# Kernel tuning notes

Measured on AMD Instinct MI355X. Metric: run time of the kernel, lower is better.

## Reference

```python
import jax, jax.numpy as jnp
import numpy as np

B, N, C, H = 8, 4096, 768, 8
EPS = 1e-12  # F.normalize eps


def setup_inputs() -> dict:
    key = jax.random.key(0)
    k1, k2, k3, k4 = jax.random.split(key, 4)
    x = jax.random.normal(k1, (B, N, C), dtype=jnp.float32)
    Wqkv = jax.random.normal(k2, (C, 3 * C), dtype=jnp.float32) * (1.0 / np.sqrt(C))
    temperature = jnp.ones((H, 1, 1), dtype=jnp.float32)
    Wproj = jax.random.normal(k3, (C, C), dtype=jnp.float32) * (1.0 / np.sqrt(C))
    bproj = jax.random.normal(k4, (C,), dtype=jnp.float32) * 0.01
    return {"x": x, "Wqkv": Wqkv, "temperature": temperature, "Wproj": Wproj, "bproj": bproj}


def _l2norm(t):
    # F.normalize(dim=-1): t / max(||t||_2, eps)
    n = jnp.sqrt(jnp.sum(t * t, axis=-1, keepdims=True))
    return t / jnp.maximum(n, EPS)


def reference(x, Wqkv, temperature, Wproj, bproj):
    b, n, c = x.shape
    h = temperature.shape[0]
    hd = c // h
    qkv = x @ Wqkv  # [B, N, 3C]
    qkv = qkv.reshape(b, n, 3, h, hd).transpose(2, 0, 3, 4, 1)  # [3, B, H, hd, N]
    q, k, v = qkv[0], qkv[1], qkv[2]
    q = _l2norm(q)  # normalize over token dim N
    k = _l2norm(k)
    # channel-channel attention: [B, H, hd, hd]
    attn = jnp.einsum('bhdn,bhen->bhde', q, k) * temperature  # temperature [H,1,1] broadcasts
    attn = jax.nn.softmax(attn, axis=-1)
    out = jnp.einsum('bhde,bhen->bhdn', attn, v)  # [B, H, hd, N]
    out = out.transpose(0, 3, 1, 2).reshape(b, n, c)  # [B, N, C]
    return out @ Wproj + bproj
```

## Files before the change

kernel.cpp:

```cpp
#include <hip/hip_runtime.h>
#include <stdint.h>


typedef __attribute__((ext_vector_type(8))) __bf16 bf16x8;
typedef __attribute__((ext_vector_type(4))) float f32x4;

__device__ __forceinline__ unsigned short f2b(float f) {
  uint32_t u = __float_as_uint(f);
  u += 0x7FFF + ((u >> 16) & 1);
  return (unsigned short)(u >> 16);
}

__device__ __forceinline__ void gload16(const void* g, void* l) {
  __builtin_amdgcn_global_load_lds(
      (__attribute__((address_space(1))) void*)(uintptr_t)g,
      (__attribute__((address_space(3))) void*)(uintptr_t)l, 16, 0, 0);
}

__global__ void cvt_bf16(const float* __restrict__ in, unsigned short* __restrict__ out, int n4,
                         float* __restrict__ Z, int nz4) {
  int gid = blockIdx.x * blockDim.x + threadIdx.x;
  if (gid < nz4) reinterpret_cast<float4*>(Z)[gid] = make_float4(0.f, 0.f, 0.f, 0.f);
  int stride = gridDim.x * blockDim.x;
  for (int i = gid; i < n4; i += stride) {
    float4 v = reinterpret_cast<const float4*>(in)[i];
    ushort4 o;
    o.x = f2b(v.x); o.y = f2b(v.y); o.z = f2b(v.z); o.w = f2b(v.w);
    reinterpret_cast<ushort4*>(out)[i] = o;
  }
}

__global__ void cvt_transpose(const float* __restrict__ in, unsigned short* __restrict__ out,
                              int K, int NC) {
  __shared__ float tile[32][33];
  int bx = blockIdx.x, by = blockIdx.y;
  int tx = threadIdx.x & 31, ty = threadIdx.x >> 5;
  for (int r = ty; r < 32; r += 8)
    tile[r][tx] = in[(size_t)(by * 32 + r) * NC + bx * 32 + tx];
  __syncthreads();
  for (int r = ty; r < 32; r += 8)
    out[(size_t)(bx * 32 + r) * K + by * 32 + tx] = f2b(tile[tx][r]);
}

__global__ __launch_bounds__(256, 2) void gemm_qkv(
    const unsigned short* __restrict__ A, const unsigned short* __restrict__ Bt,
    unsigned short* __restrict__ qkT, unsigned short* __restrict__ vT,
    float* __restrict__ normsq) {
  __shared__ __align__(16) unsigned short lds[17408];
  int bj = blockIdx.x;
  int bm = blockIdx.y;
  int m0 = bm * 128, j0 = bj * 128;
  int tid = threadIdx.x;
  int wid = tid >> 6, lane = tid & 63;
  int wm = wid >> 1, wn = wid & 1;
  int quad = lane >> 4, l16 = lane & 15;
  int srow = lane >> 3, sch = lane & 7;
  int cmem = sch ^ srow;

  f32x4 acc[4][4];
  f32x4 z = {0.f, 0.f, 0.f, 0.f};
#pragma unroll
  for (int i = 0; i < 4; i++)
#pragma unroll
    for (int j = 0; j < 4; j++) acc[i][j] = z;

  const unsigned short* Ab = A + (size_t)m0 * 768;
  const unsigned short* Bb = Bt + (size_t)j0 * 768;

  for (int k0 = 0; k0 < 768; k0 += 64) {
#pragma unroll
    for (int i = 0; i < 4; i++) {
      int ig = wid * 4 + i;
      int row = ig * 8 + srow;
      gload16(Ab + (size_t)row * 768 + k0 + cmem * 8, &lds[ig * 512]);
      gload16(Bb + (size_t)row * 768 + k0 + cmem * 8, &lds[8192 + ig * 512]);
    }
    __syncthreads();
#pragma unroll
    for (int kk = 0; kk < 2; kk++) {
      int cs = ((kk * 4 + quad) ^ (l16 & 7)) * 8;
      bf16x8 af[4], bfr[4];
#pragma unroll
      for (int mi = 0; mi < 4; mi++)
        af[mi] = *(const bf16x8*)&lds[(wm * 64 + mi * 16 + l16) * 64 + cs];
#pragma unroll
      for (int ni = 0; ni < 4; ni++)
        bfr[ni] = *(const bf16x8*)&lds[8192 + (wn * 64 + ni * 16 + l16) * 64 + cs];
#pragma unroll
      for (int mi = 0; mi < 4; mi++)
#pragma unroll
        for (int ni = 0; ni < 4; ni++)
          acc[mi][ni] = __builtin_amdgcn_mfma_f32_16x16x32_bf16(af[mi], bfr[ni], acc[mi][ni], 0, 0, 0);
    }
    __syncthreads();
  }

  int s = bj / 6;
  int b = bm >> 5;
  int n0 = m0 & 4095;
  bool isv = (s == 2);

  if (!isv) {
#pragma unroll
    for (int ni = 0; ni < 4; ni++) {
      float ss = 0.f;
#pragma unroll
      for (int mi = 0; mi < 4; mi++)
#pragma unroll
        for (int r = 0; r < 4; r++) ss += acc[mi][ni][r] * acc[mi][ni][r];
      ss += __shfl_down(ss, 32, 64);
      ss += __shfl_down(ss, 16, 64);
      if (lane < 16) {
        int cc = wn * 64 + ni * 16 + l16;
        int local = j0 + cc - s * 768;
        int hh = local / 96, d = local - hh * 96;
        atomicAdd(&normsq[s * 6144 + (b * 8 + hh) * 96 + d], ss);
      }
    }
  }

#pragma unroll
  for (int mi = 0; mi < 4; mi++)
#pragma unroll
    for (int ni = 0; ni < 4; ni++)
#pragma unroll
      for (int r = 0; r < 4; r++) {
        int m = wm * 64 + mi * 16 + quad * 4 + r;
        int cc = wn * 64 + ni * 16 + l16;
        unsigned short v = f2b(acc[mi][ni][r]);
        lds[isv ? (m * 136 + cc) : (cc * 136 + m)] = v;
      }
  __syncthreads();
  if (!isv) {
#pragma unroll
    for (int it = 0; it < 8; it++) {
      int id = tid + it * 256;
      int jr = id >> 4, mc = id & 15;
      int j = j0 + jr;
      int hh = (j - s * 768) / 96;
      int d = j - s * 768 - hh * 96;
      size_t off = ((size_t)(s * 64 + b * 8 + hh) * 96 + d) * 4096 + n0 + mc * 8;
      *(uint4*)&qkT[off] = *(const uint4*)&lds[jr * 136 + mc * 8];
    }
  } else {
#pragma unroll
    for (int it = 0; it < 8; it++) {
      int id = tid + it * 256;
      int mr = id >> 4, ch = id & 15;
      int cp = (j0 - 1536) + ch * 8;
      int hh = cp / 96, e = cp - hh * 96;
      size_t off = ((size_t)(b * 8 + hh) * 4096 + (n0 + mr)) * 96 + e;
      *(uint4*)&vT[off] = *(const uint4*)&lds[mr * 136 + ch * 8];
    }
  }
}

__global__ __launch_bounds__(256, 2) void attn_s(const unsigned short* __restrict__ qkT,
                                                 float* __restrict__ S) {
  __shared__ __align__(16) unsigned short lds[12288];
  int blk = blockIdx.x;
  int bh = blk >> 3, ks = blk & 7;
  const unsigned short* qb = qkT + (size_t)bh * 96 * 4096;
  const unsigned short* kb = qkT + (size_t)(64 + bh) * 96 * 4096;
  int tid = threadIdx.x, wid = tid >> 6, lane = tid & 63;
  int wm = wid >> 1, wn = wid & 1, quad = lane >> 4, l16 = lane & 15;
  int srow = lane >> 3, sch = lane & 7;
  int cmem = sch ^ srow;
  f32x4 acc[3][3];
  f32x4 z = {0.f, 0.f, 0.f, 0.f};
#pragma unroll
  for (int i = 0; i < 3; i++)
#pragma unroll
    for (int j = 0; j < 3; j++) acc[i][j] = z;

  for (int k0 = ks * 512; k0 < ks * 512 + 512; k0 += 64) {
#pragma unroll
    for (int i = 0; i < 3; i++) {
      int ig = wid * 3 + i;
      int row = ig * 8 + srow;
      gload16(qb + (size_t)row * 4096 + k0 + cmem * 8, &lds[ig * 512]);
      gload16(kb + (size_t)row * 4096 + k0 + cmem * 8, &lds[6144 + ig * 512]);
    }
    __syncthreads();
#pragma unroll
    for (int kk = 0; kk < 2; kk++) {
      int cs = ((kk * 4 + quad) ^ (l16 & 7)) * 8;
      bf16x8 af[3], bfr[3];
#pragma unroll
      for (int mi = 0; mi < 3; mi++)
        af[mi] = *(const bf16x8*)&lds[(wm * 48 + mi * 16 + l16) * 64 + cs];
#pragma unroll
      for (int ni = 0; ni < 3; ni++)
        bfr[ni] = *(const bf16x8*)&lds[6144 + (wn * 48 + ni * 16 + l16) * 64 + cs];
#pragma unroll
      for (int mi = 0; mi < 3; mi++)
#pragma unroll
        for (int ni = 0; ni < 3; ni++)
          acc[mi][ni] = __builtin_amdgcn_mfma_f32_16x16x32_bf16(af[mi], bfr[ni], acc[mi][ni], 0, 0, 0);
    }
    __syncthreads();
  }
  float* Sb = S + (size_t)bh * 9216;
#pragma unroll
  for (int mi = 0; mi < 3; mi++)
#pragma unroll
    for (int ni = 0; ni < 3; ni++)
#pragma unroll
      for (int r = 0; r < 4; r++)
        atomicAdd(&Sb[(wm * 48 + mi * 16 + quad * 4 + r) * 96 + wn * 48 + ni * 16 + l16],
                  acc[mi][ni][r]);
}

__global__ __launch_bounds__(128) void softmax96(
    const float* __restrict__ S, const float* __restrict__ normsq,
    const float* __restrict__ temp, unsigned short* __restrict__ attnB) {
  __shared__ float ik[96];
  int bh = blockIdx.x;
  int h = bh & 7;
  int tid = threadIdx.x;
  if (tid < 96) ik[tid] = 1.0f / fmaxf(sqrtf(normsq[6144 + bh * 96 + tid]), 1e-12f);
  __syncthreads();
  if (tid < 96) {
    int d = tid;
    const float* Srow = S + (size_t)bh * 9216 + d * 96;
    float iq = (1.0f / fmaxf(sqrtf(normsq[bh * 96 + d]), 1e-12f)) * temp[h];
    float mx = -1e30f;
    for (int e = 0; e < 96; e++) mx = fmaxf(mx, Srow[e] * iq * ik[e]);
    float sum = 0.f;
    for (int e = 0; e < 96; e++) sum += __expf(Srow[e] * iq * ik[e] - mx);
    float inv = 1.0f / sum;
    unsigned short* row = attnB + (size_t)bh * 9984 + d * 104;
    for (int e = 0; e < 96; e++) row[e] = f2b(__expf(Srow[e] * iq * ik[e] - mx) * inv);
    for (int e = 96; e < 104; e++) row[e] = 0;
  }
}

__global__ __launch_bounds__(256, 2) void attn_v(
    const unsigned short* __restrict__ attnB, const unsigned short* __restrict__ vT,
    unsigned short* __restrict__ U) {
  __shared__ __align__(16) unsigned short lds[23552];
  int blk = blockIdx.x;
  int bh = blk >> 5, nc = blk & 31;
  int b = bh >> 3, h = bh & 7;
  int n0 = nc * 128;
  int tid = threadIdx.x, wid = tid >> 6, lane = tid & 63;
  int wm = wid >> 1, wn = wid & 1, quad = lane >> 4, l16 = lane & 15;

  const unsigned short* ab = attnB + (size_t)bh * 9984;
#pragma unroll
  for (int i = 0; i < 5; i++) {
    int id = i * 256 + tid;
    int ids = id < 1248 ? id : 1247;
    gload16(ab + (size_t)ids * 8, &lds[(i * 4 + wid) * 512]);
  }

  const unsigned short* vb = vT + (size_t)bh * 4096 * 96 + (size_t)n0 * 96;
#pragma unroll
  for (int i = 0; i < 7; i++) {
    int ig = wid + i * 4;
    if (ig < 26) {
      int id = ig * 64 + lane;
      int row = id / 13;
      int ch = id - row * 13;
      if (ch > 11) ch = 11;
      gload16(vb + (size_t)row * 96 + ch * 8, &lds[10240 + ig * 512]);
    }
  }
  __syncthreads();

  f32x4 acc[3][4];
  f32x4 z = {0.f, 0.f, 0.f, 0.f};
#pragma unroll
  for (int i = 0; i < 3; i++)
#pragma unroll
    for (int j = 0; j < 4; j++) acc[i][j] = z;
#pragma unroll
  for (int et = 0; et < 3; et++) {
    bf16x8 af[3], bfr[4];
#pragma unroll
    for (int mi = 0; mi < 3; mi++)
      af[mi] = *(const bf16x8*)&lds[(wm * 48 + mi * 16 + l16) * 104 + (et * 4 + quad) * 8];
#pragma unroll
    for (int ni = 0; ni < 4; ni++)
      bfr[ni] = *(const bf16x8*)&lds[10240 + (wn * 64 + ni * 16 + l16) * 104 + (et * 4 + quad) * 8];
#pragma unroll
    for (int mi = 0; mi < 3; mi++)
#pragma unroll
      for (int ni = 0; ni < 4; ni++)
        acc[mi][ni] = __builtin_amdgcn_mfma_f32_16x16x32_bf16(af[mi], bfr[ni], acc[mi][ni], 0, 0, 0);
  }
  __syncthreads();

#pragma unroll
  for (int mi = 0; mi < 3; mi++)
#pragma unroll
    for (int ni = 0; ni < 4; ni++)
#pragma unroll
      for (int r = 0; r < 4; r++) {
        int d = wm * 48 + mi * 16 + quad * 4 + r;
        int n = wn * 64 + ni * 16 + l16;
        lds[n * 104 + d] = f2b(acc[mi][ni][r]);
      }
  __syncthreads();
#pragma unroll
  for (int it = 0; it < 6; it++) {
    int id = tid + it * 256;
    int nr = id / 12, ch = id - nr * 12;
    *(uint4*)&U[((size_t)(b * 4096 + n0 + nr)) * 768 + h * 96 + ch * 8] =
        *(const uint4*)&lds[nr * 104 + ch * 8];
  }
}

__global__ __launch_bounds__(256, 2) void gemm_out(
    const unsigned short* __restrict__ A, const unsigned short* __restrict__ Bt,
    const float* __restrict__ bias, float* __restrict__ out) {
  __shared__ __align__(16) unsigned short lds[16384];
  int bj = blockIdx.x;
  int bm = blockIdx.y;
  int m0 = bm * 128, j0 = bj * 128;
  int tid = threadIdx.x;
  int wid = tid >> 6, lane = tid & 63;
  int wm = wid >> 1, wn = wid & 1;
  int quad = lane >> 4, l16 = lane & 15;
  int srow = lane >> 3, sch = lane & 7;
  int cmem = sch ^ srow;

  f32x4 acc[4][4];
  f32x4 z = {0.f, 0.f, 0.f, 0.f};
#pragma unroll
  for (int i = 0; i < 4; i++)
#pragma unroll
    for (int j = 0; j < 4; j++) acc[i][j] = z;

  const unsigned short* Ab = A + (size_t)m0 * 768;
  const unsigned short* Bb = Bt + (size_t)j0 * 768;

  for (int k0 = 0; k0 < 768; k0 += 64) {
#pragma unroll
    for (int i = 0; i < 4; i++) {
      int ig = wid * 4 + i;
      int row = ig * 8 + srow;
      gload16(Ab + (size_t)row * 768 + k0 + cmem * 8, &lds[ig * 512]);
      gload16(Bb + (size_t)row * 768 + k0 + cmem * 8, &lds[8192 + ig * 512]);
    }
    __syncthreads();
#pragma unroll
    for (int kk = 0; kk < 2; kk++) {
      int cs = ((kk * 4 + quad) ^ (l16 & 7)) * 8;
      bf16x8 af[4], bfr[4];
#pragma unroll
      for (int mi = 0; mi < 4; mi++)
        af[mi] = *(const bf16x8*)&lds[(wm * 64 + mi * 16 + l16) * 64 + cs];
#pragma unroll
      for (int ni = 0; ni < 4; ni++)
        bfr[ni] = *(const bf16x8*)&lds[8192 + (wn * 64 + ni * 16 + l16) * 64 + cs];
#pragma unroll
      for (int mi = 0; mi < 4; mi++)
#pragma unroll
        for (int ni = 0; ni < 4; ni++)
          acc[mi][ni] = __builtin_amdgcn_mfma_f32_16x16x32_bf16(af[mi], bfr[ni], acc[mi][ni], 0, 0, 0);
    }
    __syncthreads();
  }
#pragma unroll
  for (int ni = 0; ni < 4; ni++) {
    int ccol = j0 + wn * 64 + ni * 16 + l16;
    float bv = bias[ccol];
#pragma unroll
    for (int mi = 0; mi < 4; mi++)
#pragma unroll
      for (int r = 0; r < 4; r++)
        out[(size_t)(m0 + wm * 64 + mi * 16 + quad * 4 + r) * 768 + ccol] = acc[mi][ni][r] + bv;
  }
}

extern "C" void kernel_launch(void* const* d_in, const int* in_sizes, int n_in,
                              void* d_out, int out_size, void* d_ws, size_t ws_size,
                              hipStream_t stream) {
  const float* x = (const float*)d_in[0];
  const float* Wqkv = (const float*)d_in[1];
  const float* temp = (const float*)d_in[2];
  const float* Wproj = (const float*)d_in[3];
  const float* bproj = (const float*)d_in[4];
  float* out = (float*)d_out;
  char* ws = (char*)d_ws;

  unsigned short* xb     = (unsigned short*)(ws);
  unsigned short* WqkvT  = (unsigned short*)(ws + 50331648);
  unsigned short* WprojT = (unsigned short*)(ws + 53870592);
  unsigned short* qkT    = (unsigned short*)(ws + 55050240);
  unsigned short* vT     = (unsigned short*)(ws + 155713536);
  unsigned short* U      = (unsigned short*)(ws + 206045184);
  float* S               = (float*)(ws + 256376832);
  float* normsq          = (float*)(ws + 258736128);
  unsigned short* attnB  = qkT;

  cvt_bf16<<<dim3(4096), dim3(256), 0, stream>>>(x, xb, 25165824 / 4, S, 150528);
  cvt_transpose<<<dim3(72, 24), dim3(256), 0, stream>>>(Wqkv, WqkvT, 768, 2304);
  cvt_transpose<<<dim3(24, 24), dim3(256), 0, stream>>>(Wproj, WprojT, 768, 768);
  gemm_qkv<<<dim3(18, 256), dim3(256), 0, stream>>>(xb, WqkvT, qkT, vT, normsq);
  attn_s<<<dim3(512), dim3(256), 0, stream>>>(qkT, S);
  softmax96<<<dim3(64), dim3(128), 0, stream>>>(S, normsq, temp, attnB);
  attn_v<<<dim3(2048), dim3(256), 0, stream>>>(attnB, vT, U);
  gemm_out<<<dim3(6, 256), dim3(256), 0, stream>>>(U, WprojT, bproj, out);
}
```

Before: 447.1 us.

## Rewrite QKV GEMM as 256x256 tiles with double-buffered ping-pong pipeline

The QKV projection GEMM now uses 256x256 output tiles with 512 threads and a double-buffered 128KB LDS. Global-to-LDS loads for upcoming k-steps are interleaved with the MFMA phases, using explicit vmcnt waits, barriers and raised scheduling priority. Blocks are also remapped so that neighbouring blocks share operands in cache. The goal is to hide load latency and raise operand reuse per tile, at the cost of more LDS and registers per block, which lowers occupancy, and a hand-tuned wait/barrier schedule that is easy to get wrong.

```diff
diff --git a/kernel.cpp b/kernel.cpp
--- a/kernel.cpp
+++ b/kernel.cpp
@@ -42,115 +42,188 @@
     out[(size_t)(bx * 32 + r) * K + by * 32 + tx] = f2b(tile[tx][r]);
 }
 
-__global__ __launch_bounds__(256, 2) void gemm_qkv(
+
+#define BARX() asm volatile("s_barrier" ::: "memory")
+#define WAITV(N) asm volatile("s_waitcnt vmcnt(" #N ")" ::: "memory")
+#define SCHED() __builtin_amdgcn_sched_barrier(0)
+
+#define STAGE(gbase, p, isB, h, t) do {                                             \
+  unsigned short* _lb = &lds[(p)*32768 + (isB)*16384 + (h)*8192 + wid*1024];        \
+  const unsigned short* _gb = (gbase) + (size_t)((h)*128 + wid*16)*768 + (t)*64 + lanegoff; \
+  gload16(_gb, _lb);                                                                \
+  gload16(_gb + 8*768, _lb + 512);                                                  \
+} while (0)
+
+#define LOAD_AF(p, mh) do {                                                         \
+  const unsigned short* _ab = &lds[(p)*32768 + (mh)*8192];                          \
+  _Pragma("unroll") for (int _mi = 0; _mi < 4; _mi++)                               \
+    _Pragma("unroll") for (int _kk = 0; _kk < 2; _kk++)                             \
+      af[_mi][_kk] = *(const bf16x8*)&_ab[(wm*64 + _mi*16 + l16)*64 + ((_kk*4+quad)^(l16&7))*8]; \
+} while (0)
+
+#define LOAD_BF(dst, p, nh) do {                                                    \
+  const unsigned short* _bb = &lds[(p)*32768 + 16384 + (nh)*8192];                  \
+  _Pragma("unroll") for (int _ni = 0; _ni < 2; _ni++)                               \
+    _Pragma("unroll") for (int _kk = 0; _kk < 2; _kk++)                             \
+      dst[_ni][_kk] = *(const bf16x8*)&_bb[(wn*32 + _ni*16 + l16)*64 + ((_kk*4+quad)^(l16&7))*8]; \
+} while (0)
+
+#define MFMA_PH(mh, nh, bfx) do {                                                   \
+  __builtin_amdgcn_s_setprio(1);                                                    \
+  _Pragma("unroll") for (int _m = 0; _m < 4; _m++)                                  \
+    _Pragma("unroll") for (int _n = 0; _n < 2; _n++)                                \
+      _Pragma("unroll") for (int _k = 0; _k < 2; _k++)                              \
+        acc[(mh)*4+_m][(nh)*2+_n] = __builtin_amdgcn_mfma_f32_16x16x32_bf16(        \
+            af[_m][_k], bfx[_n][_k], acc[(mh)*4+_m][(nh)*2+_n], 0, 0, 0);           \
+  __builtin_amdgcn_s_setprio(0);                                                    \
+} while (0)
+
+__global__ __launch_bounds__(512, 2) void gemm_qkv(
     const unsigned short* __restrict__ A, const unsigned short* __restrict__ Bt,
     unsigned short* __restrict__ qkT, unsigned short* __restrict__ vT,
     float* __restrict__ normsq) {
-  __shared__ __align__(16) unsigned short lds[17408];
-  int bj = blockIdx.x;
-  int bm = blockIdx.y;
-  int m0 = bm * 128, j0 = bj * 128;
+  __shared__ __align__(16) unsigned short lds[65536];
+  int lin = blockIdx.y * 9 + blockIdx.x;
+  int swz = (lin & 7) * 144 + (lin >> 3);
+  int bm = swz / 9;
+  int bj = swz - bm * 9;
+  int m0 = bm * 256, j0 = bj * 256;
   int tid = threadIdx.x;
   int wid = tid >> 6, lane = tid & 63;
-  int wm = wid >> 1, wn = wid & 1;
+  int wm = wid >> 2, wn = wid & 3;
   int quad = lane >> 4, l16 = lane & 15;
   int srow = lane >> 3, sch = lane & 7;
   int cmem = sch ^ srow;
-
-  f32x4 acc[4][4];
+  int lanegoff = srow * 768 + cmem * 8;
+
+  f32x4 acc[8][4];
   f32x4 z = {0.f, 0.f, 0.f, 0.f};
 #pragma unroll
-  for (int i = 0; i < 4; i++)
+  for (int i = 0; i < 8; i++)
 #pragma unroll
     for (int j = 0; j < 4; j++) acc[i][j] = z;
 
-  const unsigned short* Ab = A + (size_t)m0 * 768;
-  const unsigned short* Bb = Bt + (size_t)j0 * 768;
-
-  for (int k0 = 0; k0 < 768; k0 += 64) {
-#pragma unroll
-    for (int i = 0; i < 4; i++) {
-      int ig = wid * 4 + i;
-      int row = ig * 8 + srow;
-      gload16(Ab + (size_t)row * 768 + k0 + cmem * 8, &lds[ig * 512]);
-      gload16(Bb + (size_t)row * 768 + k0 + cmem * 8, &lds[8192 + ig * 512]);
-    }
-    __syncthreads();
-#pragma unroll
-    for (int kk = 0; kk < 2; kk++) {
-      int cs = ((kk * 4 + quad) ^ (l16 & 7)) * 8;
-      bf16x8 af[4], bfr[4];
-#pragma unroll
-      for (int mi = 0; mi < 4; mi++)
-        af[mi] = *(const bf16x8*)&lds[(wm * 64 + mi * 16 + l16) * 64 + cs];
-#pragma unroll
-      for (int ni = 0; ni < 4; ni++)
-        bfr[ni] = *(const bf16x8*)&lds[8192 + (wn * 64 + ni * 16 + l16) * 64 + cs];
-#pragma unroll
-      for (int mi = 0; mi < 4; mi++)
-#pragma unroll
-        for (int ni = 0; ni < 4; ni++)
-          acc[mi][ni] = __builtin_amdgcn_mfma_f32_16x16x32_bf16(af[mi], bfr[ni], acc[mi][ni], 0, 0, 0);
-    }
-    __syncthreads();
-  }
-
-  int s = bj / 6;
-  int b = bm >> 5;
+  bf16x8 af[4][2], bf0[2][2], bf1[2][2];
+
+  const unsigned short* Ab2 = A + (size_t)m0 * 768;
+  const unsigned short* Bb2 = Bt + (size_t)j0 * 768;
+
+  STAGE(Ab2, 0, 0, 0, 0); STAGE(Bb2, 0, 1, 0, 0); STAGE(Bb2, 0, 1, 1, 0); STAGE(Ab2, 0, 0, 1, 0);
+  STAGE(Ab2, 1, 0, 0, 1); STAGE(Bb2, 1, 1, 0, 1); STAGE(Bb2, 1, 1, 1, 1); STAGE(Ab2, 1, 0, 1, 1);
+  WAITV(12);
+  BARX();
+
+  for (int t = 0; t < 10; t++) {
+    int p = t & 1;
+    LOAD_AF(p, 0); LOAD_BF(bf0, p, 0);
+    if (t >= 1) STAGE(Ab2, p ^ 1, 0, 1, t + 1);
+    BARX(); SCHED();
+    MFMA_PH(0, 0, bf0);
+    SCHED(); WAITV(10); BARX();
+    LOAD_BF(bf1, p, 1);
+    STAGE(Ab2, p, 0, 0, t + 2);
+    BARX(); SCHED();
+    MFMA_PH(0, 1, bf1);
+    SCHED(); WAITV(10); BARX();
+    LOAD_AF(p, 1);
+    STAGE(Bb2, p, 1, 0, t + 2);
+    BARX(); SCHED();
+    MFMA_PH(1, 1, bf1);
+    SCHED(); BARX();
+    STAGE(Bb2, p, 1, 1, t + 2);
+    BARX(); SCHED();
+    MFMA_PH(1, 0, bf0);
+    SCHED(); WAITV(10); BARX();
+  }
+  LOAD_AF(0, 0); LOAD_BF(bf0, 0, 0);
+  STAGE(Ab2, 1, 0, 1, 11);
+  BARX(); SCHED(); MFMA_PH(0, 0, bf0); SCHED(); WAITV(10); BARX();
+  LOAD_BF(bf1, 0, 1);
+  BARX(); SCHED(); MFMA_PH(0, 1, bf1); SCHED(); WAITV(8); BARX();
+  LOAD_AF(0, 1);
+  BARX(); SCHED(); MFMA_PH(1, 1, bf1); SCHED(); BARX();
+  BARX(); SCHED(); MFMA_PH(1, 0, bf0); SCHED(); WAITV(4); BARX();
+  LOAD_AF(1, 0); LOAD_BF(bf0, 1, 0);
+  BARX(); SCHED(); MFMA_PH(0, 0, bf0); SCHED(); WAITV(2); BARX();
+  LOAD_BF(bf1, 1, 1);
+  BARX(); SCHED(); MFMA_PH(0, 1, bf1); SCHED(); WAITV(0); BARX();
+  LOAD_AF(1, 1);
+  BARX(); SCHED(); MFMA_PH(1, 1, bf1); SCHED(); BARX();
+  BARX(); SCHED(); MFMA_PH(1, 0, bf0); SCHED(); BARX();
+
+  int s = bj / 3;
+  int b = m0 >> 12;
   int n0 = m0 & 4095;
-  bool isv = (s == 2);
-
-  if (!isv) {
+
+  if (s < 2) {
 #pragma unroll
     for (int ni = 0; ni < 4; ni++) {
       float ss = 0.f;
 #pragma unroll
-      for (int mi = 0; mi < 4; mi++)
+      for (int mi = 0; mi < 8; mi++)
 #pragma unroll
         for (int r = 0; r < 4; r++) ss += acc[mi][ni][r] * acc[mi][ni][r];
       ss += __shfl_down(ss, 32, 64);
       ss += __shfl_down(ss, 16, 64);
       if (lane < 16) {
-        int cc = wn * 64 + ni * 16 + l16;
+        int cc = (ni >> 1) * 128 + wn * 32 + (ni & 1) * 16 + l16;
         int local = j0 + cc - s * 768;
         int hh = local / 96, d = local - hh * 96;
         atomicAdd(&normsq[s * 6144 + (b * 8 + hh) * 96 + d], ss);
       }
     }
-  }
-
-#pragma unroll
-  for (int mi = 0; mi < 4; mi++)
-#pragma unroll
-    for (int ni = 0; ni < 4; ni++)
-#pragma unroll
-      for (int r = 0; r < 4; r++) {
-        int m = wm * 64 + mi * 16 + quad * 4 + r;
-        int cc = wn * 64 + ni * 16 + l16;
-        unsigned short v = f2b(acc[mi][ni][r]);
-        lds[isv ? (m * 136 + cc) : (cc * 136 + m)] = v;
-      }
-  __syncthreads();
-  if (!isv) {
-#pragma unroll
-    for (int it = 0; it < 8; it++) {
-      int id = tid + it * 256;
-      int jr = id >> 4, mc = id & 15;
-      int j = j0 + jr;
-      int hh = (j - s * 768) / 96;
-      int d = j - s * 768 - hh * 96;
-      size_t off = ((size_t)(s * 64 + b * 8 + hh) * 96 + d) * 4096 + n0 + mc * 8;
-      *(uint4*)&qkT[off] = *(const uint4*)&lds[jr * 136 + mc * 8];
+#pragma unroll
+    for (int jh = 0; jh < 2; jh++) {
+      __syncthreads();
+#pragma unroll
+      for (int nl = 0; nl < 2; nl++) {
+        int ni = jh * 2 + nl;
+        int jc = wn * 32 + nl * 16 + l16;
+#pragma unroll
+        for (int mi = 0; mi < 8; mi++) {
+          int mrow = (mi >> 2) * 128 + wm * 64 + (mi & 3) * 16 + quad * 4;
+#pragma unroll
+          for (int r = 0; r < 4; r++) lds[jc * 264 + mrow + r] = f2b(acc[mi][ni][r]);
+        }
+      }
+      __syncthreads();
+#pragma unroll
+      for (int it = 0; it < 8; it++) {
+        int id = it * 512 + tid;
+        int jr = id >> 5, mc = id & 31;
+        int j = j0 + jh * 128 + jr;
+        int local = j - s * 768;
+        int hh = local / 96, d = local - hh * 96;
+        size_t off = ((size_t)(s * 64 + b * 8 + hh) * 96 + d) * 4096 + n0 + mc * 8;
+        *(uint4*)&qkT[off] = *(const uint4*)&lds[jr * 264 + mc * 8];
+      }
     }
   } else {
-#pragma unroll
-    for (int it = 0; it < 8; it++) {
-      int id = tid + it * 256;
-      int mr = id >> 4, ch = id & 15;
-      int cp = (j0 - 1536) + ch * 8;
-      int hh = cp / 96, e = cp - hh * 96;
-      size_t off = ((size_t)(b * 8 + hh) * 4096 + (n0 + mr)) * 96 + e;
-      *(uint4*)&vT[off] = *(const uint4*)&lds[mr * 136 + ch * 8];
+    int j0v = j0 - 1536;
+#pragma unroll
+    for (int mh = 0; mh < 2; mh++) {
+      __syncthreads();
+#pragma unroll
+      for (int ml = 0; ml < 4; ml++) {
+        int mi = mh * 4 + ml;
+        int mloc = wm * 64 + ml * 16 + quad * 4;
+#pragma unroll
+        for (int ni = 0; ni < 4; ni++) {
+          int jc = (ni >> 1) * 128 + wn * 32 + (ni & 1) * 16 + l16;
+#pragma unroll
+          for (int r = 0; r < 4; r++) lds[(mloc + r) * 264 + jc] = f2b(acc[mi][ni][r]);
+        }
+      }
+      __syncthreads();
+#pragma unroll
+      for (int it = 0; it < 8; it++) {
+        int id = it * 512 + tid;
+        int mr = id >> 5, ch = id & 31;
+        int cp = j0v + ch * 8;
+        int hh = cp / 96, e = cp - hh * 96;
+        size_t off = ((size_t)(b * 8 + hh) * 4096 + (n0 + mh * 128 + mr)) * 96 + e;
+        *(uint4*)&vT[off] = *(const uint4*)&lds[mr * 264 + ch * 8];
+      }
     }
   }
 }
@@ -398,7 +471,7 @@
   cvt_bf16<<<dim3(4096), dim3(256), 0, stream>>>(x, xb, 25165824 / 4, S, 150528);
   cvt_transpose<<<dim3(72, 24), dim3(256), 0, stream>>>(Wqkv, WqkvT, 768, 2304);
   cvt_transpose<<<dim3(24, 24), dim3(256), 0, stream>>>(Wproj, WprojT, 768, 768);
-  gemm_qkv<<<dim3(18, 256), dim3(256), 0, stream>>>(xb, WqkvT, qkT, vT, normsq);
+  gemm_qkv<<<dim3(9, 128), dim3(512), 0, stream>>>(xb, WqkvT, qkT, vT, normsq);
   attn_s<<<dim3(512), dim3(256), 0, stream>>>(qkT, S);
   softmax96<<<dim3(64), dim3(128), 0, stream>>>(S, normsq, temp, attnB);
   attn_v<<<dim3(2048), dim3(256), 0, stream>>>(attnB, vT, U);
```

Measured after the change: 442.6 us. About the same (-1.0%).
